# Kernel tuning notes

Hardware: AMD Instinct MI355X
Metric: run time of the kernel (lower is better)

## Reference

```python
import jax, jax.numpy as jnp
import numpy as np

B, C, H, W, K = 8, 64, 96, 96, 4
D = 2 * C + 1  # 129 = fg/bg feats + query feats + cosine channel
EPS_COV = 1e-6
LOG2PI = float(np.log(2.0 * np.pi))


def _bn(x, g, b):
    # BatchNorm2d in training mode: batch stats over (B,H,W), biased var, eps=1e-5
    m = x.mean(axis=(0, 2, 3), keepdims=True)
    v = x.var(axis=(0, 2, 3), keepdims=True)
    return (x - m) / jnp.sqrt(v + 1e-5) * g[None, :, None, None] + b[None, :, None, None]


def _conv1x1(x, w, b):
    return jnp.einsum('bchw,cd->bdhw', x, w) + b[None, :, None, None]


def _estimator(x, p):
    w1, b1, g1, be1, w2, b2, g2, be2, w3, b3 = p
    h = jax.nn.relu(_bn(_conv1x1(x, w1, b1), g1, be1))
    h = jax.nn.relu(_bn(_conv1x1(h, w2, b2), g2, be2))
    return jax.nn.softmax(_conv1x1(h, w3, b3), axis=1)  # soft assignment over K


def _cosine(a, b):
    num = (a * b).sum(axis=1)
    na = jnp.sqrt((a * a).sum(axis=1))
    nb = jnp.sqrt((b * b).sum(axis=1))
    return num / (jnp.maximum(na, 1e-8) * jnp.maximum(nb, 1e-8))


def _gmm(z, gamma):
    # DAGMM-style phi / mean / cov / sample energy
    b, d, h, w = z.shape
    n = h * w
    zf = z.reshape(b, d, n).transpose(0, 2, 1)      # [B,N,D]
    gm = gamma.reshape(b, K, n).transpose(0, 2, 1)  # [B,N,K]
    sum_g = gm.sum(axis=1)                          # [B,K]
    phi = sum_g / n
    mu = jnp.einsum('bnk,bnd->bkd', gm, zf) / sum_g[:, :, None]          # [B,K,D]
    diff = zf[:, None, :, :] - mu[:, :, None, :]                         # [B,K,N,D]
    cov = jnp.einsum('bnk,bknd,bkne->bkde', gm, diff, diff) / sum_g[:, :, None, None]
    cov = cov + EPS_COV * jnp.eye(d, dtype=z.dtype)
    L = jnp.linalg.cholesky(cov)                                         # [B,K,D,D]
    y = jax.scipy.linalg.solve_triangular(L, diff.transpose(0, 1, 3, 2), lower=True)  # [B,K,D,N]
    quad = (y * y).sum(axis=2)                                           # [B,K,N]
    logdet = 2.0 * jnp.log(jnp.diagonal(L, axis1=-2, axis2=-1)).sum(-1)  # [B,K]
    logp = -0.5 * quad - 0.5 * (logdet + d * LOG2PI)[:, :, None] + jnp.log(phi + 1e-12)[:, :, None]
    energy = -jax.scipy.special.logsumexp(logp, axis=1).mean()
    return phi, mu, L, energy


def _sample(phi, mu, L, noise):
    # MVN(mu, cov) reparameterized sample scaled by phi, vectorized over (B,K)
    return (mu + jnp.einsum('bkde,bke->bkd', L, noise)) * phi[:, :, None]


def setup_inputs() -> dict:
    key = jax.random.key(0)
    ks = jax.random.split(key, 10)
    inp = {
        'support_feature': jax.random.normal(ks[0], (B, C, H, W), jnp.float32),
        'support_mask': jax.random.uniform(ks[1], (B, 1, H, W), jnp.float32),
        'query_feature': jax.random.normal(ks[2], (B, C, H, W), jnp.float32),
        'w1': jax.random.normal(ks[3], (D, 64), jnp.float32) * 0.01,
        'b1': jnp.zeros((64,), jnp.float32),
        'g1': jnp.ones((64,), jnp.float32),
        'be1': jnp.zeros((64,), jnp.float32),
        'w2': jax.random.normal(ks[4], (64, 16), jnp.float32) * 0.01,
        'b2': jnp.zeros((16,), jnp.float32),
        'g2': jnp.ones((16,), jnp.float32),
        'be2': jnp.zeros((16,), jnp.float32),
        'w3': jax.random.normal(ks[5], (16, K), jnp.float32) * 0.01,
        'b3': jnp.zeros((K,), jnp.float32),
        'noise_fg': jax.random.normal(ks[6], (B, K, D), jnp.float32),
        'noise_bg': jax.random.normal(ks[7], (B, K, D), jnp.float32),
    }
    return inp


def reference(support_feature, support_mask, query_feature,
              w1, b1, g1, be1, w2, b2, g2, be2, w3, b3,
              noise_fg, noise_bg):
    # mask already at feature resolution -> bilinear resize is identity
    mask = support_mask
    fg = support_feature * mask
    bg = support_feature * (1.0 - mask)
    cf = _cosine(fg, query_feature)
    cb = _cosine(bg, query_feature)
    z_fg = jnp.concatenate([fg, query_feature, cf[:, None]], axis=1)  # [B,D,H,W]
    z_bg = jnp.concatenate([bg, query_feature, cb[:, None]], axis=1)
    p = (w1, b1, g1, be1, w2, b2, g2, be2, w3, b3)
    gamma_fg = _estimator(z_fg, p)
    gamma_bg = _estimator(z_bg, p)
    phi_f, mu_f, L_f, e_f = _gmm(z_fg, gamma_fg)
    phi_b, mu_b, L_b, e_b = _gmm(z_bg, gamma_bg)
    fs_f = _sample(phi_f, mu_f, L_f, noise_fg)  # [B,K,D]
    fs_b = _sample(phi_b, mu_b, L_b, noise_bg)
    # mu_ list -> stacked [K,B,D,1,1]
    mu_stack = jnp.transpose(fs_f, (1, 0, 2))[..., None, None]
    # discriminative model
    b, d, h, w = z_fg.shape
    zf = z_fg.reshape(b, d, h * w)                        # [B,D,N]
    mu_cat = jnp.concatenate([fs_f, fs_b], axis=1)        # [B,2K,D]
    logits = jnp.einsum('bdn,bmd->bnm', zf, mu_cat)       # [B,N,2K]
    P = jax.nn.softmax(logits, axis=2).transpose(0, 2, 1).reshape(b, 2 * K, h, w)
    P_f = P[:, :K].sum(axis=1, keepdims=True)
    P_b = P[:, K:].sum(axis=1, keepdims=True)
    Prob_map = jnp.concatenate([P_b, P_f], axis=1)        # [B,2,H,W]
    return (mu_stack, Prob_map, e_f, e_b)
```

## Files before the change

### kernel.cpp

```cpp
#include <hip/hip_runtime.h>
#include <math.h>

#define NPIX 9216
#define NBATCH 8
#define NC 64
#define ND 129
#define NK 4
#define NCOMBO 64
#define PITCH 132
#define APITCH 131
#define WPACK 8976


__device__ __forceinline__ const float* zrow(const float* fgbg, const float* cfcb, const float* qf,
                                             int br, int b, int d){
  if(d < NC)        return fgbg + ((size_t)((br*NBATCH + b)*NC + d))*NPIX;
  else if(d < 2*NC) return qf   + ((size_t)(b*NC + (d - NC)))*NPIX;
  else              return cfcb + (size_t)(br*NBATCH + b)*NPIX;
}

__device__ __forceinline__ float blockSum256(float v, float* rb){
  int tid = threadIdx.x;
  rb[tid] = v; __syncthreads();
  #pragma unroll
  for(int s = 128; s > 0; s >>= 1){
    if(tid < s) rb[tid] += rb[tid + s];
    __syncthreads();
  }
  float r = rb[0]; __syncthreads();
  return r;
}


__global__ __launch_bounds__(256) void k_prep(const float* sf, const float* smk, const float* qf,
                                              float* fgbg, float* cfcb){
  int tid = threadIdx.x, b = blockIdx.y;
  int n = blockIdx.x*256 + tid;
  float m = smk[(size_t)b*NPIX + n];
  const float* S = sf + ((size_t)(b*NC))*NPIX + n;
  const float* Q = qf + ((size_t)(b*NC))*NPIX + n;
  float* FG = fgbg + ((size_t)(b*NC))*NPIX + n;
  float* BG = fgbg + ((size_t)((NBATCH + b)*NC))*NPIX + n;
  float df = 0.f, db = 0.f, nf = 0.f, nb_ = 0.f, nq = 0.f;
  #pragma unroll 4
  for(int c = 0; c < NC; c++){
    float s = S[(size_t)c*NPIX], q = Q[(size_t)c*NPIX];
    float f = s*m, g = s - f;
    FG[(size_t)c*NPIX] = f; BG[(size_t)c*NPIX] = g;
    df += f*q; db += g*q; nf += f*f; nb_ += g*g; nq += q*q;
  }
  float rq = fmaxf(sqrtf(nq), 1e-8f);
  cfcb[(size_t)b*NPIX + n]            = df / (fmaxf(sqrtf(nf),  1e-8f) * rq);
  cfcb[(size_t)(NBATCH + b)*NPIX + n] = db / (fmaxf(sqrtf(nb_), 1e-8f) * rq);
}


__global__ __launch_bounds__(256) void k_conv1(const float* fgbg, const float* cfcb, const float* qf,
                                               const float* w1, const float* b1, float* h1){
  __shared__ float Ws[ND*NC];
  __shared__ float B1[NC];
  int tid = threadIdx.x, b = blockIdx.y, br = blockIdx.z;
  for(int i = tid; i < ND*NC; i += 256) Ws[i] = w1[i];
  if(tid < NC) B1[tid] = b1[tid];
  __syncthreads();
  int n = blockIdx.x*256 + tid;
  float acc[NC];
  #pragma unroll
  for(int j = 0; j < NC; j++) acc[j] = B1[j];
  const float* Z0 = fgbg + ((size_t)((br*NBATCH + b)*NC))*NPIX + n;
  #pragma unroll 2
  for(int d = 0; d < NC; d++){
    float z = Z0[(size_t)d*NPIX];
    #pragma unroll
    for(int j = 0; j < NC; j++) acc[j] += z*Ws[d*NC + j];
  }
  const float* Q = qf + ((size_t)(b*NC))*NPIX + n;
  #pragma unroll 2
  for(int d = 0; d < NC; d++){
    float z = Q[(size_t)d*NPIX];
    #pragma unroll
    for(int j = 0; j < NC; j++) acc[j] += z*Ws[(NC + d)*NC + j];
  }
  {
    float z = cfcb[(size_t)(br*NBATCH + b)*NPIX + n];
    #pragma unroll
    for(int j = 0; j < NC; j++) acc[j] += z*Ws[128*NC + j];
  }
  float* O = h1 + ((size_t)((br*NBATCH + b)*NC))*NPIX + n;
  #pragma unroll
  for(int j = 0; j < NC; j++) O[(size_t)j*NPIX] = acc[j];
}

__global__ __launch_bounds__(256) void k_bnpart(const float* x, float* part, int C){
  __shared__ float rb[256];
  int c = blockIdx.x, br = blockIdx.y, b = blockIdx.z, tid = threadIdx.x;
  const float4* X = (const float4*)(x + ((size_t)((br*NBATCH + b)*C + c))*NPIX);
  float s = 0.f, ss = 0.f;
  for(int n = tid; n < NPIX/4; n += 256){
    float4 v = X[n];
    s  += v.x + v.y + v.z + v.w;
    ss += v.x*v.x + v.y*v.y + v.z*v.z + v.w*v.w;
  }
  float S  = blockSum256(s,  rb);
  float SS = blockSum256(ss, rb);
  if(tid == 0){
    atomicAdd(&part[(size_t)(br*C + c)*2],     S);
    atomicAdd(&part[(size_t)(br*C + c)*2 + 1], SS);
  }
}

__global__ void k_bnfin(const float* part, float* meanv, float* rstdv, int C){
  int i = blockIdx.x*64 + threadIdx.x;
  if(i < 2*C){
    float m = part[(size_t)i*2]     / (float)(NBATCH*NPIX);
    float v = part[(size_t)i*2 + 1] / (float)(NBATCH*NPIX) - m*m;
    meanv[i] = m;
    rstdv[i] = 1.0f / sqrtf(v + 1e-5f);
  }
}

__global__ __launch_bounds__(256) void k_conv2(const float* h1, const float* mean1, const float* rstd1,
                                               const float* g1, const float* be1,
                                               const float* w2, const float* b2, float* h2){
  __shared__ float Ws[NC*16];
  __shared__ float Pm[NC], Pr[NC], Pg[NC], Pb[NC];
  __shared__ float B2[16];
  int tid = threadIdx.x, b = blockIdx.y, br = blockIdx.z;
  for(int i = tid; i < NC*16; i += 256) Ws[i] = w2[i];
  if(tid < NC){ Pm[tid] = mean1[br*NC + tid]; Pr[tid] = rstd1[br*NC + tid]; Pg[tid] = g1[tid]; Pb[tid] = be1[tid]; }
  if(tid < 16) B2[tid] = b2[tid];
  __syncthreads();
  int n = blockIdx.x*256 + tid;
  const float* X = h1 + ((size_t)((br*NBATCH + b)*NC))*NPIX + n;
  float acc[16];
  #pragma unroll
  for(int j = 0; j < 16; j++) acc[j] = B2[j];
  for(int c = 0; c < NC; c++){
    float v = (X[(size_t)c*NPIX] - Pm[c])*Pr[c]*Pg[c] + Pb[c];
    v = fmaxf(v, 0.f);
    #pragma unroll
    for(int j = 0; j < 16; j++) acc[j] += v*Ws[c*16 + j];
  }
  float* O = h2 + ((size_t)((br*NBATCH + b)*16))*NPIX + n;
  #pragma unroll
  for(int j = 0; j < 16; j++) O[(size_t)j*NPIX] = acc[j];
}

__global__ __launch_bounds__(256) void k_gamma(const float* h2, const float* mean2, const float* rstd2,
                                               const float* g2, const float* be2,
                                               const float* w3, const float* b3,
                                               float* gamma, float* sumg){
  __shared__ float W3[16*4];
  __shared__ float Pm[16], Pr[16], Pg[16], Pb[16];
  __shared__ float B3[4];
  __shared__ float rb[256];
  int tid = threadIdx.x, b = blockIdx.y, br = blockIdx.z;
  if(tid < 64) W3[tid] = w3[tid];
  if(tid < 4)  B3[tid] = b3[tid];
  if(tid < 16){ Pm[tid] = mean2[br*16 + tid]; Pr[tid] = rstd2[br*16 + tid]; Pg[tid] = g2[tid]; Pb[tid] = be2[tid]; }
  __syncthreads();
  int n = blockIdx.x*256 + tid;
  const float* X = h2 + ((size_t)((br*NBATCH + b)*16))*NPIX + n;
  float l0 = B3[0], l1 = B3[1], l2 = B3[2], l3 = B3[3];
  #pragma unroll
  for(int c = 0; c < 16; c++){
    float v = (X[(size_t)c*NPIX] - Pm[c])*Pr[c]*Pg[c] + Pb[c];
    v = fmaxf(v, 0.f);
    l0 += v*W3[c*4 + 0]; l1 += v*W3[c*4 + 1]; l2 += v*W3[c*4 + 2]; l3 += v*W3[c*4 + 3];
  }
  float mx = fmaxf(fmaxf(l0, l1), fmaxf(l2, l3));
  float e0 = expf(l0 - mx), e1 = expf(l1 - mx), e2 = expf(l2 - mx), e3 = expf(l3 - mx);
  float inv = 1.0f / (e0 + e1 + e2 + e3);
  float q0 = e0*inv, q1 = e1*inv, q2 = e2*inv, q3 = e3*inv;
  float* G = gamma + ((size_t)((br*NBATCH + b)*NK))*NPIX + n;
  G[0] = q0; G[NPIX] = q1; G[2*NPIX] = q2; G[3*NPIX] = q3;
  int cb = br*NBATCH + b;
  float t;
  t = blockSum256(q0, rb); if(tid == 0) atomicAdd(&sumg[cb*4 + 0], t);
  t = blockSum256(q1, rb); if(tid == 0) atomicAdd(&sumg[cb*4 + 1], t);
  t = blockSum256(q2, rb); if(tid == 0) atomicAdd(&sumg[cb*4 + 2], t);
  t = blockSum256(q3, rb); if(tid == 0) atomicAdd(&sumg[cb*4 + 3], t);
}


__global__ __launch_bounds__(256) void k_musum(const float* fgbg, const float* cfcb, const float* qf,
                                               const float* gamma, float* musum){
  __shared__ float rb[256];
  int d = blockIdx.x, b = blockIdx.y, br = blockIdx.z, tid = threadIdx.x;
  const float* Z = zrow(fgbg, cfcb, qf, br, b, d);
  const float* G = gamma + ((size_t)((br*NBATCH + b)*NK))*NPIX;
  float a0 = 0.f, a1 = 0.f, a2 = 0.f, a3 = 0.f;
  for(int n = tid; n < NPIX; n += 256){
    float z = Z[n];
    a0 += G[n]*z; a1 += G[NPIX + n]*z; a2 += G[2*NPIX + n]*z; a3 += G[3*NPIX + n]*z;
  }
  int cb = br*NBATCH + b;
  float t;
  t = blockSum256(a0, rb); if(tid == 0) musum[((size_t)(cb*4 + 0))*ND + d] = t;
  t = blockSum256(a1, rb); if(tid == 0) musum[((size_t)(cb*4 + 1))*ND + d] = t;
  t = blockSum256(a2, rb); if(tid == 0) musum[((size_t)(cb*4 + 2))*ND + d] = t;
  t = blockSum256(a3, rb); if(tid == 0) musum[((size_t)(cb*4 + 3))*ND + d] = t;
}

__global__ __launch_bounds__(256) void k_phimufin(const float* sumg, float* phi, float* logphi, float* mu){
  int tid = threadIdx.x;
  if(tid < NCOMBO){
    float sg = sumg[tid];
    float p = sg / (float)NPIX;
    phi[tid] = p;
    logphi[tid] = logf(p + 1e-12f);
  }
  for(int i = tid; i < NCOMBO*ND; i += 256){
    int c = i / ND;
    mu[i] = mu[i] / sumg[c];
  }
}


__global__ __launch_bounds__(256) void k_cov(const float* fgbg, const float* cfcb, const float* qf,
                                             const float* gamma, float* Mpart){
  __shared__ float SD[32][34];
  __shared__ float SE[32][34];
  __shared__ __align__(16) float SG[32][4];
  int p = blockIdx.x, cbi = blockIdx.y, seg = blockIdx.z;
  int ti, tj;
  if(p < 4){ ti = 0; tj = p; } else if(p < 7){ ti = 1; tj = p - 3; }
  else if(p < 9){ ti = 2; tj = p - 5; } else { ti = 3; tj = 3; }
  int br = cbi >> 3, b = cbi & 7;
  int d0 = ti*32, e0 = tj*32;
  int tid = threadIdx.x, tx = tid & 15, ty = tid >> 4;
  float at[2][2] = {{0,0},{0,0}}, a0[2][2] = {{0,0},{0,0}}, a1[2][2] = {{0,0},{0,0}}, a2[2][2] = {{0,0},{0,0}};
  const float* G = gamma + ((size_t)(cbi*NK))*NPIX;
  int r = tid >> 3, jj = (tid & 7)*4;
  const float* Zd = zrow(fgbg, cfcb, qf, br, b, d0 + r);
  const float* Ze = zrow(fgbg, cfcb, qf, br, b, e0 + r);
  for(int nc = 0; nc < 72; nc++){
    int n0 = seg*2304 + nc*32;
    __syncthreads();
    {
      float4 v = *(const float4*)(Zd + n0 + jj);
      SD[jj][r] = v.x; SD[jj+1][r] = v.y; SD[jj+2][r] = v.z; SD[jj+3][r] = v.w;
      v = *(const float4*)(Ze + n0 + jj);
      SE[jj][r] = v.x; SE[jj+1][r] = v.y; SE[jj+2][r] = v.z; SE[jj+3][r] = v.w;
      if(tid < 128) SG[tid & 31][tid >> 5] = G[(size_t)(tid >> 5)*NPIX + n0 + (tid & 31)];
    }
    __syncthreads();
    #pragma unroll 4
    for(int nn = 0; nn < 32; nn++){
      float4 g4 = *(const float4*)(&SG[nn][0]);
      float zd0 = SD[nn][2*ty], zd1 = SD[nn][2*ty + 1];
      float ze0 = SE[nn][2*tx], ze1 = SE[nn][2*tx + 1];
      #pragma unroll
      for(int i = 0; i < 2; i++){
        float zd = i ? zd1 : zd0;
        #pragma unroll
        for(int j = 0; j < 2; j++){
          float ze = j ? ze1 : ze0;
          float pr = zd*ze;
          at[i][j] += pr;
          a0[i][j] += g4.x*pr;
          a1[i][j] += g4.y*pr;
          a2[i][j] += g4.z*pr;
        }
      }
    }
  }
  size_t slot0 = (size_t)(seg*64 + cbi*4);
  size_t st = (size_t)ND*PITCH;
  #pragma unroll
  for(int i = 0; i < 2; i++){
    #pragma unroll
    for(int j = 0; j < 2; j++){
      int d = d0 + 2*ty + i, e = e0 + 2*tx + j;
      if(e >= d){
        size_t o = (slot0*ND + d)*PITCH + e;
        Mpart[o]        = a0[i][j];
        Mpart[o + st]   = a1[i][j];
        Mpart[o + 2*st] = a2[i][j];
        Mpart[o + 3*st] = at[i][j];
      }
    }
  }
}

__global__ __launch_bounds__(256) void k_covstrip(const float* fgbg, const float* cfcb, const float* qf,
                                                  const float* gamma, float* Mpart){
  __shared__ float rb[256];
  int e = blockIdx.x, cb = blockIdx.y, seg = blockIdx.z, tid = threadIdx.x;
  int br = cb >> 3, b = cb & 7;
  const float* Ze = zrow(fgbg, cfcb, qf, br, b, e);
  const float* CF = cfcb + (size_t)cb*NPIX;
  const float* G  = gamma + ((size_t)(cb*NK))*NPIX;
  float at = 0.f, a0 = 0.f, a1 = 0.f, a2 = 0.f;
  int n0 = seg*2304;
  for(int n = n0 + tid; n < n0 + 2304; n += 256){
    float pr = Ze[n]*CF[n];
    at += pr; a0 += G[n]*pr; a1 += G[NPIX + n]*pr; a2 += G[2*NPIX + n]*pr;
  }
  size_t base = ((size_t)(seg*64 + cb*4)*ND + e)*PITCH + 128;
  size_t st = (size_t)ND*PITCH;
  float t;
  t = blockSum256(a0, rb); if(tid == 0) Mpart[base]        = t;
  t = blockSum256(a1, rb); if(tid == 0) Mpart[base + st]   = t;
  t = blockSum256(a2, rb); if(tid == 0) Mpart[base + 2*st] = t;
  t = blockSum256(at, rb); if(tid == 0) Mpart[base + 3*st] = t;
}

__global__ __launch_bounds__(192) void k_covfin(const float* Mpart, const float* sumg, const float* mu,
                                                float* covb){
  int i = blockIdx.x, c = blockIdx.y, j = threadIdx.x;
  if(j > i) return;
  int k = c & 3, cb4 = c & ~3;
  size_t st = (size_t)ND*PITCH;
  float s = 0.f;
  if(k < 3){
    #pragma unroll
    for(int sg = 0; sg < 4; sg++) s += Mpart[((size_t)(sg*64 + c)*ND + j)*PITCH + i];
  } else {
    #pragma unroll
    for(int sg = 0; sg < 4; sg++){
      size_t base = ((size_t)(sg*64 + cb4)*ND + j)*PITCH + i;
      s += Mpart[base + 3*st] - Mpart[base] - Mpart[base + st] - Mpart[base + 2*st];
    }
  }
  float sgv = sumg[c];
  float v = s/sgv - mu[(size_t)c*ND + i]*mu[(size_t)c*ND + j];
  if(i == j) v += 1e-6f;
  covb[((size_t)c*ND + i)*PITCH + j] = v;
}


__global__ __launch_bounds__(256) void k_cholinv(const float* covb, const float* muv, const float* phiv,
                                                 const float* nzf, const float* nzb,
                                                 float* Wpk, float* logdet, float* fs, float* dout){
  extern __shared__ float sh[];
  float* A    = sh;
  float* Wl   = sh + ND*APITCH;
  float* rs   = Wl + ND*ND;
  float* cbuf = rs + 132;
  __shared__ float rb[256];
  int c = blockIdx.x, tid = threadIdx.x;
  for(int idx = tid; idx < ND*ND; idx += 256){
    int i = idx / ND, j = idx - i*ND;
    if(j <= i) A[i*APITCH + j] = covb[((size_t)c*ND + i)*PITCH + j];
  }
  if(tid == 0) cbuf[0] = 1.0f / A[0];
  __syncthreads();
  for(int j = 0; j < ND-1; j++){
    float invd = cbuf[j & 1];
    int i = j + 1 + tid;
    if(i < ND){
      float* Ai = A + (size_t)i*APITCH;
      float f = Ai[j] * invd;
      const float* Cj = A + j;
      #pragma unroll 4
      for(int k = j + 1; k <= i; k++) Ai[k] -= f * Cj[(size_t)k*APITCH];
      if(tid == 0) cbuf[(j + 1) & 1] = 1.0f / Ai[j + 1];
    }
    __syncthreads();
  }
  if(tid < ND) rs[tid] = 1.0f / sqrtf(A[(size_t)tid*APITCH + tid]);
  __syncthreads();
  for(int idx = tid; idx < ND*ND; idx += 256){
    int i = idx / ND, j = idx - i*ND;
    if(j <= i) A[(size_t)i*APITCH + j] *= rs[j];
  }
  __syncthreads();
  float ld = (tid < ND) ? logf(A[(size_t)tid*APITCH + tid]) : 0.f;
  float lsum = blockSum256(ld, rb);
  if(tid == 0) logdet[c] = 2.f*lsum;
  int br = c >> 5, b = (c >> 2) & 7, kk = c & 3;
  const float* nz = (br ? nzb : nzf) + (size_t)(b*NK + kk)*ND;
  if(tid < ND){
    const float* Ar = A + (size_t)tid*APITCH;
    float s = muv[(size_t)c*ND + tid];
    #pragma unroll 4
    for(int e = 0; e <= tid; e++) s += Ar[e]*nz[e];
    float v = s*phiv[c];
    fs[(size_t)c*ND + tid] = v;
    if(br == 0) dout[(size_t)kk*(NBATCH*ND) + (size_t)b*ND + tid] = v;
  }
  {
    int cc = tid;
    float* Wc = Wl + (size_t)cc*ND;
    for(int i = 0; i < ND; i++){
      if(cc <= i && cc < ND){
        float s = (i == cc) ? 1.f : 0.f;
        const float* Ar = A + (size_t)i*APITCH;
        #pragma unroll 4
        for(int k = cc; k < i; k++) s -= Ar[k]*Wc[k];
        Wc[i] = s * rs[i];
      }
    }
  }
  __syncthreads();
  {
    float* dst0 = Wpk + (size_t)c*WPACK;
    int S = 0;
    for(int e = 0; e < 132; e++){
      int dstart = e & ~3;
      float* dst = dst0 + S;
      for(int i = dstart + tid; i < 132; i += 256){
        float v = 0.f;
        if(e < ND && i >= e && i < ND) v = Wl[(size_t)e*ND + i];
        dst[i - dstart] = v;
      }
      S += 132 - dstart;
    }
  }
}


#define QFMA(acc, wv) \
  acc.x += (wv)*x.x; acc.y += (wv)*x.y; acc.z += (wv)*x.z; acc.w += (wv)*x.w;

__global__ __launch_bounds__(256) void k_quad(const float* fgbg, const float* cfcb, const float* qf,
                                              const float* Wp, const float* mu, float* quad){
  extern __shared__ float sh[];
  float* DF = sh;
  int c = blockIdx.y;
  int br = c >> 5, b = (c >> 2) & 7;
  int n0 = blockIdx.x*64;
  int tid = threadIdx.x;
  for(int idx = tid; idx < 132*16; idx += 256){
    int r = idx >> 4, c4 = (idx & 15)*4;
    float4 v = make_float4(0.f, 0.f, 0.f, 0.f);
    if(r < ND){
      const float* Zr = zrow(fgbg, cfcb, qf, br, b, r);
      v = *(const float4*)(Zr + n0 + c4);
      float m = mu[(size_t)c*ND + r];
      v.x -= m; v.y -= m; v.z -= m; v.w -= m;
    }
    *(float4*)&DF[r*68 + c4] = v;
  }
  __syncthreads();
  const float4* Wc4 = (const float4*)(Wp + (size_t)c*WPACK);
  int tx = tid & 15, ty = tid >> 4;
  int p0 = 4*tx;
  float4 q = make_float4(0.f, 0.f, 0.f, 0.f);
  #pragma unroll
  for(int P = 0; P < 2; P++){
    int d0 = 4*(16*P + ty);
    bool fat = (P == 1) && (ty == 15);
    int eA = min(d0 + 4, ND);
    float4 A0 = make_float4(0,0,0,0), A1 = A0, A2 = A0, A3 = A0;
    float4 B0 = A0, B1 = A0, B2 = A0, B3 = A0;
    int base4 = d0 >> 2;
    #pragma unroll 4
    for(int e = 0; e < eA; e++){
      float4 x = *(const float4*)&DF[e*68 + p0];
      float4 w = Wc4[base4];
      QFMA(A0, w.x) QFMA(A1, w.y) QFMA(A2, w.z) QFMA(A3, w.w)
      if(fat){
        float4 w2 = Wc4[base4 + 1];
        QFMA(B0, w2.x) QFMA(B1, w2.y) QFMA(B2, w2.z) QFMA(B3, w2.w)
      }
      base4 += 33 - (e >> 2) - (((e & 3) == 3) ? 1 : 0);
    }
    if(fat){
      base4 += 1;
      for(int e = eA; e < ND; e++){
        float4 x = *(const float4*)&DF[e*68 + p0];
        float4 w2 = Wc4[base4];
        QFMA(B0, w2.x) QFMA(B1, w2.y) QFMA(B2, w2.z) QFMA(B3, w2.w)
        base4 += 33 - (e >> 2) - (((e & 3) == 3) ? 1 : 0);
      }
    }
    q.x += A0.x*A0.x + A1.x*A1.x + A2.x*A2.x + A3.x*A3.x;
    q.y += A0.y*A0.y + A1.y*A1.y + A2.y*A2.y + A3.y*A3.y;
    q.z += A0.z*A0.z + A1.z*A1.z + A2.z*A2.z + A3.z*A3.z;
    q.w += A0.w*A0.w + A1.w*A1.w + A2.w*A2.w + A3.w*A3.w;
    if(fat){
      q.x += B0.x*B0.x + B1.x*B1.x + B2.x*B2.x + B3.x*B3.x;
      q.y += B0.y*B0.y + B1.y*B1.y + B2.y*B2.y + B3.y*B3.y;
      q.z += B0.z*B0.z + B1.z*B1.z + B2.z*B2.z + B3.z*B3.z;
      q.w += B0.w*B0.w + B1.w*B1.w + B2.w*B2.w + B3.w*B3.w;
    }
  }
  __syncthreads();
  float* QR = sh;
  *(float4*)&QR[ty*68 + p0] = q;
  __syncthreads();
  if(tid < 64){
    float s = 0.f;
    #pragma unroll
    for(int t = 0; t < 16; t++) s += QR[t*68 + tid];
    quad[(size_t)c*NPIX + n0 + tid] = s;
  }
}


__global__ __launch_bounds__(256) void k_energy(const float* quad, const float* logdet, const float* logphi,
                                                float* eacc){
  __shared__ float rb[256];
  int tid = threadIdx.x;
  int n = blockIdx.x*256 + tid, b = blockIdx.y, br = blockIdx.z;
  int c0 = (br*NBATCH + b)*NK;
  const float C0 = 118.54307078340277f;
  float l0 = -0.5f*quad[(size_t)(c0 + 0)*NPIX + n] - 0.5f*logdet[c0 + 0] - C0 + logphi[c0 + 0];
  float l1 = -0.5f*quad[(size_t)(c0 + 1)*NPIX + n] - 0.5f*logdet[c0 + 1] - C0 + logphi[c0 + 1];
  float l2 = -0.5f*quad[(size_t)(c0 + 2)*NPIX + n] - 0.5f*logdet[c0 + 2] - C0 + logphi[c0 + 2];
  float l3 = -0.5f*quad[(size_t)(c0 + 3)*NPIX + n] - 0.5f*logdet[c0 + 3] - C0 + logphi[c0 + 3];
  float mx = fmaxf(fmaxf(l0, l1), fmaxf(l2, l3));
  float lse = mx + logf(expf(l0 - mx) + expf(l1 - mx) + expf(l2 - mx) + expf(l3 - mx));
  float t = blockSum256(lse, rb);
  if(tid == 0) atomicAdd(&eacc[br], t);
}

__global__ void k_fin(const float* eacc, float* dout){
  int t = threadIdx.x;
  if(t < 2) dout[151584 + t] = -eacc[t] / (float)(NBATCH*NPIX);
}


__global__ __launch_bounds__(256) void k_prob(const float* fgbg, const float* cfcb, const float* qf,
                                              const float* fs, float* dout){
  __shared__ float MC[8][132];
  int b = blockIdx.y, tid = threadIdx.x;
  for(int idx = tid; idx < 8*ND; idx += 256){
    int m = idx / ND, d = idx - m*ND;
    int br = m >> 2, kk = m & 3;
    MC[m][d] = fs[(size_t)((br*NBATCH + b)*NK + kk)*ND + d];
  }
  __syncthreads();
  int n = blockIdx.x*256 + tid;
  float a[8] = {0,0,0,0,0,0,0,0};
  const float* Z0 = fgbg + ((size_t)(b*NC))*NPIX + n;
  for(int d = 0; d < NC; d++){
    float z = Z0[(size_t)d*NPIX];
    #pragma unroll
    for(int m = 0; m < 8; m++) a[m] += z*MC[m][d];
  }
  const float* Q = qf + ((size_t)(b*NC))*NPIX + n;
  for(int d = 0; d < NC; d++){
    float z = Q[(size_t)d*NPIX];
    #pragma unroll
    for(int m = 0; m < 8; m++) a[m] += z*MC[m][NC + d];
  }
  {
    float z = cfcb[(size_t)b*NPIX + n];
    #pragma unroll
    for(int m = 0; m < 8; m++) a[m] += z*MC[m][128];
  }
  float mx = a[0];
  #pragma unroll
  for(int m = 1; m < 8; m++) mx = fmaxf(mx, a[m]);
  float e[8]; float ssum = 0.f;
  #pragma unroll
  for(int m = 0; m < 8; m++){ e[m] = expf(a[m] - mx); ssum += e[m]; }
  float inv = 1.f/ssum;
  float Pf = (e[0] + e[1] + e[2] + e[3])*inv;
  float Pb = (e[4] + e[5] + e[6] + e[7])*inv;
  dout[4128 + ((size_t)(b*2))*NPIX + n]     = Pb;
  dout[4128 + ((size_t)(b*2 + 1))*NPIX + n] = Pf;
}


extern "C" void kernel_launch(void* const* d_in, const int* in_sizes, int n_in,
                              void* d_out, int out_size, void* d_ws, size_t ws_size,
                              hipStream_t stream){
  const float* sf  = (const float*)d_in[0];
  const float* smk = (const float*)d_in[1];
  const float* qfp = (const float*)d_in[2];
  const float* w1  = (const float*)d_in[3];
  const float* b1  = (const float*)d_in[4];
  const float* g1  = (const float*)d_in[5];
  const float* be1 = (const float*)d_in[6];
  const float* w2  = (const float*)d_in[7];
  const float* b2  = (const float*)d_in[8];
  const float* g2  = (const float*)d_in[9];
  const float* be2 = (const float*)d_in[10];
  const float* w3  = (const float*)d_in[11];
  const float* b3  = (const float*)d_in[12];
  const float* nzf = (const float*)d_in[13];
  const float* nzb = (const float*)d_in[14];
  float* out = (float*)d_out;
  float* W   = (float*)d_ws;

  constexpr size_t OFF_FGBG  = 0;
  constexpr size_t SZ_FGBG   = (size_t)2*NBATCH*NC*NPIX;
  constexpr size_t OFF_CFCB  = OFF_FGBG + SZ_FGBG;
  constexpr size_t SZ_CFCB   = (size_t)2*NBATCH*NPIX;
  constexpr size_t OFF_H1    = OFF_CFCB + SZ_CFCB;
  constexpr size_t SZ_H1     = (size_t)2*NBATCH*NC*NPIX;
  constexpr size_t OFF_MPART = OFF_H1;
  constexpr size_t SZ_MPART  = (size_t)4*NCOMBO*ND*PITCH;
  constexpr size_t OFF_COVB  = OFF_H1 + SZ_MPART;
  constexpr size_t OFF_H2    = OFF_H1 + SZ_H1;
  constexpr size_t SZ_H2     = (size_t)2*NBATCH*16*NPIX;
  constexpr size_t OFF_W     = OFF_H2;
  constexpr size_t OFF_GAMMA = OFF_H2 + SZ_H2;
  constexpr size_t SZ_GAMMA  = (size_t)2*NBATCH*NK*NPIX;
  constexpr size_t OFF_QUAD  = OFF_GAMMA + SZ_GAMMA;
  constexpr size_t SZ_QUAD   = SZ_GAMMA;
  constexpr size_t OFF_SC    = OFF_QUAD + SZ_QUAD;

  float* fgbg  = W + OFF_FGBG;
  float* cfcb  = W + OFF_CFCB;
  float* h1    = W + OFF_H1;
  float* h2    = W + OFF_H2;
  float* gamma = W + OFF_GAMMA;
  float* quad  = W + OFF_QUAD;
  float* Mpart = W + OFF_MPART;
  float* covb  = W + OFF_COVB;
  float* Wpack = W + OFF_W;
  float* sc    = W + OFF_SC;
  float* mean1 = sc;          float* rstd1  = sc + 128;
  float* mean2 = sc + 256;    float* rstd2  = sc + 288;
  float* sumg  = sc + 320;    float* eacc   = sc + 384;
  float* bnp1  = sc + 386;    float* bnp2   = sc + 642;
  float* phi   = sc + 706;    float* logphi = sc + 770;
  float* mu    = sc + 834;
  float* logdetv = sc + 9090;
  float* fsv   = sc + 9154;

  hipMemsetAsync(sumg, 0, 386*sizeof(float), stream);

  k_prep   <<<dim3(36, 8),      256, 0, stream>>>(sf, smk, qfp, fgbg, cfcb);
  k_conv1  <<<dim3(36, 8, 2),   256, 0, stream>>>(fgbg, cfcb, qfp, w1, b1, h1);
  k_bnpart <<<dim3(64, 2, 8),   256, 0, stream>>>(h1, bnp1, 64);
  k_bnfin  <<<2, 64,                0, stream>>>(bnp1, mean1, rstd1, 64);
  k_conv2  <<<dim3(36, 8, 2),   256, 0, stream>>>(h1, mean1, rstd1, g1, be1, w2, b2, h2);
  k_bnpart <<<dim3(16, 2, 8),   256, 0, stream>>>(h2, bnp2, 16);
  k_bnfin  <<<1, 64,                0, stream>>>(bnp2, mean2, rstd2, 16);
  k_gamma  <<<dim3(36, 8, 2),   256, 0, stream>>>(h2, mean2, rstd2, g2, be2, w3, b3, gamma, sumg);
  k_musum  <<<dim3(129, 8, 2),  256, 0, stream>>>(fgbg, cfcb, qfp, gamma, mu);
  k_phimufin<<<1,               256, 0, stream>>>(sumg, phi, logphi, mu);
  k_cov    <<<dim3(10, 16, 4),  256, 0, stream>>>(fgbg, cfcb, qfp, gamma, Mpart);
  k_covstrip<<<dim3(129, 16, 4),256, 0, stream>>>(fgbg, cfcb, qfp, gamma, Mpart);
  k_covfin <<<dim3(129, 64),    192, 0, stream>>>(Mpart, sumg, mu, covb);
  k_cholinv<<<64, 256, (ND*APITCH + ND*ND + 132 + 4)*sizeof(float), stream>>>(covb, mu, phi, nzf, nzb,
                                                                              Wpack, logdetv, fsv, out);
  k_quad   <<<dim3(144, 64),    256, (132*68)*sizeof(float), stream>>>(
                                     fgbg, cfcb, qfp, Wpack, mu, quad);
  k_energy <<<dim3(36, 8, 2),   256, 0, stream>>>(quad, logdetv, logphi, eacc);
  k_prob   <<<dim3(36, 8),      256, 0, stream>>>(fgbg, cfcb, qfp, fsv, out);
  k_fin    <<<1, 64, 0, stream>>>(eacc, out);
}
```

Baseline: 1.394 ms.

## Block the in-LDS Cholesky factorization into rank-4 panel updates

New measurement: 1.241 ms. 11.0% less time.

```diff
diff --git a/kernel.cpp b/kernel.cpp
--- a/kernel.cpp
+++ b/kernel.cpp
@@ -8,7 +8,8 @@
 #define NK 4
 #define NCOMBO 64
 #define PITCH 132
-#define APITCH 131
+#define CAP 132
+#define CWP 130
 #define WPACK 8976
 
 
@@ -335,44 +336,84 @@
                                                  float* Wpk, float* logdet, float* fs, float* dout){
   extern __shared__ float sh[];
   float* A    = sh;
-  float* Wl   = sh + ND*APITCH;
-  float* rs   = Wl + ND*ND;
-  float* cbuf = rs + 132;
+  float* Wl   = sh + ND*CAP;
+  float* rs   = Wl + ND*CWP;
+  float* dbuf = rs + 132;
   __shared__ float rb[256];
   int c = blockIdx.x, tid = threadIdx.x;
   for(int idx = tid; idx < ND*ND; idx += 256){
     int i = idx / ND, j = idx - i*ND;
-    if(j <= i) A[i*APITCH + j] = covb[((size_t)c*ND + i)*PITCH + j];
-  }
-  if(tid == 0) cbuf[0] = 1.0f / A[0];
-  __syncthreads();
-  for(int j = 0; j < ND-1; j++){
-    float invd = cbuf[j & 1];
-    int i = j + 1 + tid;
-    if(i < ND){
-      float* Ai = A + (size_t)i*APITCH;
-      float f = Ai[j] * invd;
-      const float* Cj = A + j;
-      #pragma unroll 4
-      for(int k = j + 1; k <= i; k++) Ai[k] -= f * Cj[(size_t)k*APITCH];
-      if(tid == 0) cbuf[(j + 1) & 1] = 1.0f / Ai[j + 1];
-    }
-    __syncthreads();
-  }
-  if(tid < ND) rs[tid] = 1.0f / sqrtf(A[(size_t)tid*APITCH + tid]);
+    if(j <= i) A[(size_t)i*CAP + j] = covb[((size_t)c*ND + i)*PITCH + j];
+  }
+  if(tid == 0) dbuf[0] = 1.0f / A[0];
+  __syncthreads();
+  for(int J = 0; J < ND; J += 4){
+    int pb = (J >> 2) & 1;
+    #pragma unroll
+    for(int l = 0; l < 3; l++){
+      int j = J + l;
+      int i = j + 1 + tid;
+      if(j < ND && i < ND){
+        float invd = (l == 0) ? dbuf[pb] : dbuf[1 + l];
+        float f = A[(size_t)i*CAP + j] * invd;
+        #pragma unroll
+        for(int m = l + 1; m < 4; m++){
+          if(J + m < ND && i >= J + m){
+            float piv = A[(size_t)(J + m)*CAP + j];
+            float nv = A[(size_t)i*CAP + (J + m)] - f*piv;
+            A[(size_t)i*CAP + (J + m)] = nv;
+            if(i == J + m && m == l + 1) dbuf[2 + l] = 1.0f / nv;
+          }
+        }
+      }
+      __syncthreads();
+    }
+    {
+      int i = J + 4 + tid;
+      if(J + 4 < ND && i < ND){
+        float i0 = dbuf[pb], i1 = dbuf[2], i2 = dbuf[3], i3 = dbuf[4];
+        float* Ai = A + (size_t)i*CAP;
+        float4 fv = *(const float4*)&Ai[J];
+        float f0 = fv.x*i0, f1 = fv.y*i1, f2 = fv.z*i2, f3 = fv.w*i3;
+        int k = J + 4;
+        int nq = (i - k + 1) >> 2;
+        for(int q = 0; q < nq; q++, k += 4){
+          float4 x  = *(const float4*)&Ai[k];
+          float4 c0 = *(const float4*)&A[(size_t)(k+0)*CAP + J];
+          float4 c1 = *(const float4*)&A[(size_t)(k+1)*CAP + J];
+          float4 c2 = *(const float4*)&A[(size_t)(k+2)*CAP + J];
+          float4 c3 = *(const float4*)&A[(size_t)(k+3)*CAP + J];
+          x.x -= f0*c0.x + f1*c0.y + f2*c0.z + f3*c0.w;
+          x.y -= f0*c1.x + f1*c1.y + f2*c1.z + f3*c1.w;
+          x.z -= f0*c2.x + f1*c2.y + f2*c2.z + f3*c2.w;
+          x.w -= f0*c3.x + f1*c3.y + f2*c3.z + f3*c3.w;
+          *(float4*)&Ai[k] = x;
+        }
+        float nv = 0.f;
+        for(; k <= i; k++){
+          float4 ck = *(const float4*)&A[(size_t)k*CAP + J];
+          nv = Ai[k] - (f0*ck.x + f1*ck.y + f2*ck.z + f3*ck.w);
+          Ai[k] = nv;
+        }
+        if(i == J + 4) dbuf[pb ^ 1] = 1.0f / nv;
+      }
+      __syncthreads();
+    }
+  }
+  if(tid < ND) rs[tid] = 1.0f / sqrtf(A[(size_t)tid*CAP + tid]);
   __syncthreads();
   for(int idx = tid; idx < ND*ND; idx += 256){
     int i = idx / ND, j = idx - i*ND;
-    if(j <= i) A[(size_t)i*APITCH + j] *= rs[j];
-  }
-  __syncthreads();
-  float ld = (tid < ND) ? logf(A[(size_t)tid*APITCH + tid]) : 0.f;
+    if(j <= i) A[(size_t)i*CAP + j] *= rs[j];
+  }
+  __syncthreads();
+  float ld = (tid < ND) ? logf(A[(size_t)tid*CAP + tid]) : 0.f;
   float lsum = blockSum256(ld, rb);
   if(tid == 0) logdet[c] = 2.f*lsum;
   int br = c >> 5, b = (c >> 2) & 7, kk = c & 3;
   const float* nz = (br ? nzb : nzf) + (size_t)(b*NK + kk)*ND;
   if(tid < ND){
-    const float* Ar = A + (size_t)tid*APITCH;
+    const float* Ar = A + (size_t)tid*CAP;
     float s = muv[(size_t)c*ND + tid];
     #pragma unroll 4
     for(int e = 0; e <= tid; e++) s += Ar[e]*nz[e];
@@ -382,11 +423,11 @@
   }
   {
     int cc = tid;
-    float* Wc = Wl + (size_t)cc*ND;
+    float* Wc = Wl + (size_t)cc*CWP;
     for(int i = 0; i < ND; i++){
       if(cc <= i && cc < ND){
         float s = (i == cc) ? 1.f : 0.f;
-        const float* Ar = A + (size_t)i*APITCH;
+        const float* Ar = A + (size_t)i*CAP;
         #pragma unroll 4
         for(int k = cc; k < i; k++) s -= Ar[k]*Wc[k];
         Wc[i] = s * rs[i];
@@ -402,7 +443,7 @@
       float* dst = dst0 + S;
       for(int i = dstart + tid; i < 132; i += 256){
         float v = 0.f;
-        if(e < ND && i >= e && i < ND) v = Wl[(size_t)e*ND + i];
+        if(e < ND && i >= e && i < ND) v = Wl[(size_t)e*CWP + i];
         dst[i - dstart] = v;
       }
       S += 132 - dstart;
@@ -629,8 +670,8 @@
   k_cov    <<<dim3(10, 16, 4),  256, 0, stream>>>(fgbg, cfcb, qfp, gamma, Mpart);
   k_covstrip<<<dim3(129, 16, 4),256, 0, stream>>>(fgbg, cfcb, qfp, gamma, Mpart);
   k_covfin <<<dim3(129, 64),    192, 0, stream>>>(Mpart, sumg, mu, covb);
-  k_cholinv<<<64, 256, (ND*APITCH + ND*ND + 132 + 4)*sizeof(float), stream>>>(covb, mu, phi, nzf, nzb,
-                                                                              Wpack, logdetv, fsv, out);
+  k_cholinv<<<64, 256, (ND*CAP + ND*CWP + 132 + 8)*sizeof(float), stream>>>(covb, mu, phi, nzf, nzb,
+                                                                            Wpack, logdetv, fsv, out);
   k_quad   <<<dim3(144, 64),    256, (132*68)*sizeof(float), stream>>>(
                                      fgbg, cfcb, qfp, Wpack, mu, quad);
   k_energy <<<dim3(36, 8, 2),   256, 0, stream>>>(quad, logdetv, logphi, eacc);
```
